# Kernel optimization log

Measured on AMD Instinct MI355X. Metric: run time of the kernel, lower is better.

## Reference

```python
import jax, jax.numpy as jnp
import numpy as np

N = 8192
F_IN, HID, LAT = 256, 128, 32


def setup_inputs() -> dict:
    key = jax.random.key(0)
    k1, k2, k3, k4 = jax.random.split(key, 4)
    X = jax.random.normal(k1, (N, F_IN), dtype=jnp.float32)
    # Dense normalized-adjacency stand-in (original converts dense A_tilde to COO each call)
    A_tilde = jax.random.uniform(k2, (N, N), dtype=jnp.float32) / N
    # Xavier-uniform init like torch's init.xavier_uniform_ on Linear weights
    lim1 = float(np.sqrt(6.0 / (F_IN + HID)))
    lim2 = float(np.sqrt(6.0 / (HID + LAT)))
    W1 = jax.random.uniform(k3, (F_IN, HID), dtype=jnp.float32, minval=-lim1, maxval=lim1)
    W2 = jax.random.uniform(k4, (HID, LAT), dtype=jnp.float32, minval=-lim2, maxval=lim2)
    return {"X": X, "A_tilde": A_tilde, "W1": W1, "W2": W2}


def reference(X, A_tilde, W1, W2):
    # GCN layer 1: A_tilde @ (X W1), then ReLU
    h = jax.nn.relu(A_tilde @ (X @ W1))          # [N, HID]
    # GCN layer 2 (no activation)
    Z = A_tilde @ (h @ W2)                        # [N, LAT]
    # Inner-product decoder
    A_hat = jax.nn.sigmoid(Z @ Z.T)               # [N, N]
    return A_hat
```

## Files before the change

kernel.cpp:

```cpp
#include <hip/hip_runtime.h>
#include <hip/hip_bf16.h>

#define N_ 8192
#define F_ 256
#define H_ 128
#define L_ 32

typedef __attribute__((ext_vector_type(8))) short bf16x8;
typedef __attribute__((ext_vector_type(4))) float f32x4;
typedef __attribute__((ext_vector_type(4))) short bf16x4;

__device__ __forceinline__ unsigned f2bf_u(float x) {
    unsigned u = __builtin_bit_cast(unsigned, x);
    return (u + 0x7fffu + ((u >> 16) & 1u)) >> 16;
}
__device__ __forceinline__ short f2bf(float x) { return (short)f2bf_u(x); }

__device__ __forceinline__ bf16x8 cvt8(float4 a, float4 b) {
    bf16x8 v;
    v[0] = f2bf(a.x); v[1] = f2bf(a.y); v[2] = f2bf(a.z); v[3] = f2bf(a.w);
    v[4] = f2bf(b.x); v[5] = f2bf(b.y); v[6] = f2bf(b.z); v[7] = f2bf(b.w);
    return v;
}

__global__ __launch_bounds__(256) void k0_cvt(const float* __restrict__ A,
                                              short* __restrict__ Ab) {
    size_t g = ((size_t)blockIdx.x * 256 + threadIdx.x) * 8;
    float4 a = *(const float4*)(A + g);
    float4 b = *(const float4*)(A + g + 4);
    *(bf16x8*)(Ab + g) = cvt8(a, b);
}

__global__ __launch_bounds__(256) void k1_xw1(const float* __restrict__ X,
                                              const float* __restrict__ W1,
                                              short* __restrict__ XW1T) {
    __shared__ short w1t[H_ * (F_ + 8)];
    const int tid = threadIdx.x;
    for (int idx = tid; idx < F_ * H_; idx += 256) {
        int k = idx >> 7, n = idx & 127;
        w1t[n * (F_ + 8) + k] = f2bf(W1[idx]);
    }
    __syncthreads();
    const int wv = tid >> 6, l = tid & 63;
    const int lm = l & 15, q = l >> 4;
    const int i0 = blockIdx.x * 64 + wv * 16;
    const float* xrow = X + (size_t)(i0 + lm) * F_;
    f32x4 acc[8];
#pragma unroll
    for (int j = 0; j < 8; ++j) acc[j] = (f32x4){0.f, 0.f, 0.f, 0.f};
#pragma unroll
    for (int k0 = 0; k0 < F_; k0 += 32) {
        float4 a0 = *(const float4*)(xrow + k0 + q * 8);
        float4 a1 = *(const float4*)(xrow + k0 + q * 8 + 4);
        bf16x8 af = cvt8(a0, a1);
#pragma unroll
        for (int j = 0; j < 8; ++j) {
            bf16x8 bf = *(const bf16x8*)&w1t[(j * 16 + lm) * (F_ + 8) + k0 + q * 8];
            acc[j] = __builtin_amdgcn_mfma_f32_16x16x32_bf16(af, bf, acc[j], 0, 0, 0);
        }
    }
#pragma unroll
    for (int j = 0; j < 8; ++j) {
        bf16x4 o;
        o[0] = f2bf(acc[j][0]); o[1] = f2bf(acc[j][1]);
        o[2] = f2bf(acc[j][2]); o[3] = f2bf(acc[j][3]);
        *(bf16x4*)(XW1T + (size_t)(j * 16 + lm) * N_ + i0 + q * 4) = o;
    }
}

__global__ __launch_bounds__(256) void k2_h_zp(const short* __restrict__ Ab,
                                               const short* __restrict__ XW1T,
                                               const float* __restrict__ W2,
                                               short* __restrict__ ZPT) {
    __shared__ float lacc[4][16][132];
    __shared__ short hl[16][136];
    __shared__ short w2t[32][136];
    const int tid = threadIdx.x;
    for (int idx = tid; idx < H_ * L_; idx += 256) {
        int k = idx >> 5, j = idx & 31;
        w2t[j][k] = f2bf(W2[idx]);
    }
    const int wv = tid >> 6, l = tid & 63, lm = l & 15, q = l >> 4;
    const int i0 = blockIdx.x * 16;
    const int kbeg = wv * (N_ / 4);
    const short* Arow = Ab + (size_t)(i0 + lm) * N_ + kbeg + q * 8;
    const short* Bp[8];
#pragma unroll
    for (int jt = 0; jt < 8; ++jt)
        Bp[jt] = XW1T + (size_t)(jt * 16 + lm) * N_ + kbeg + q * 8;

    bf16x8 pa[2], pb[2][8];
#pragma unroll
    for (int t = 0; t < 2; ++t) {
        pa[t] = *(const bf16x8*)(Arow + t * 32);
#pragma unroll
        for (int jt = 0; jt < 8; ++jt) pb[t][jt] = *(const bf16x8*)(Bp[jt] + t * 32);
    }
    f32x4 acc[8];
#pragma unroll
    for (int j = 0; j < 8; ++j) acc[j] = (f32x4){0.f, 0.f, 0.f, 0.f};

    const int NS = (N_ / 4) / 32;
#pragma unroll 2
    for (int s = 0; s < NS; ++s) {
        const int p = s & 1;
        bf16x8 af = pa[p];
#pragma unroll
        for (int jt = 0; jt < 8; ++jt)
            acc[jt] = __builtin_amdgcn_mfma_f32_16x16x32_bf16(af, pb[p][jt], acc[jt], 0, 0, 0);
        if (s + 2 < NS) {
            pa[p] = *(const bf16x8*)(Arow + (s + 2) * 32);
#pragma unroll
            for (int jt = 0; jt < 8; ++jt)
                pb[p][jt] = *(const bf16x8*)(Bp[jt] + (s + 2) * 32);
        }
    }
#pragma unroll
    for (int jt = 0; jt < 8; ++jt)
#pragma unroll
        for (int r = 0; r < 4; ++r)
            lacc[wv][q * 4 + r][jt * 16 + lm] = acc[jt][r];
    __syncthreads();
    for (int e = tid; e < 16 * H_; e += 256) {
        int rr = e >> 7, c = e & 127;
        float v = (lacc[0][rr][c] + lacc[1][rr][c]) + (lacc[2][rr][c] + lacc[3][rr][c]);
        hl[rr][c] = f2bf(v > 0.f ? v : 0.f);
    }
    __syncthreads();
    if (wv < 2) {
        f32x4 a2 = (f32x4){0.f, 0.f, 0.f, 0.f};
#pragma unroll
        for (int k0 = 0; k0 < H_; k0 += 32) {
            bf16x8 af2 = *(const bf16x8*)&hl[lm][k0 + q * 8];
            bf16x8 bf2 = *(const bf16x8*)&w2t[wv * 16 + lm][k0 + q * 8];
            a2 = __builtin_amdgcn_mfma_f32_16x16x32_bf16(af2, bf2, a2, 0, 0, 0);
        }
        bf16x4 o;
        o[0] = f2bf(a2[0]); o[1] = f2bf(a2[1]); o[2] = f2bf(a2[2]); o[3] = f2bf(a2[3]);
        *(bf16x4*)(ZPT + (size_t)(wv * 16 + lm) * N_ + i0 + q * 4) = o;
    }
}

__global__ __launch_bounds__(256) void k3_z(const short* __restrict__ Ab,
                                            const short* __restrict__ ZPT,
                                            short* __restrict__ Z) {
    __shared__ float lacc[4][16][36];
    const int tid = threadIdx.x;
    const int wv = tid >> 6, l = tid & 63, lm = l & 15, q = l >> 4;
    const int i0 = blockIdx.x * 16;
    const int kbeg = wv * (N_ / 4);
    const short* Arow = Ab + (size_t)(i0 + lm) * N_ + kbeg + q * 8;
    const short* Bp0 = ZPT + (size_t)lm * N_ + kbeg + q * 8;
    const short* Bp1 = Bp0 + (size_t)16 * N_;

    bf16x8 pa[2], pb0[2], pb1[2];
#pragma unroll
    for (int t = 0; t < 2; ++t) {
        pa[t]  = *(const bf16x8*)(Arow + t * 32);
        pb0[t] = *(const bf16x8*)(Bp0 + t * 32);
        pb1[t] = *(const bf16x8*)(Bp1 + t * 32);
    }
    f32x4 acc0 = (f32x4){0.f, 0.f, 0.f, 0.f};
    f32x4 acc1 = (f32x4){0.f, 0.f, 0.f, 0.f};
    const int NS = (N_ / 4) / 32;
#pragma unroll 2
    for (int s = 0; s < NS; ++s) {
        const int p = s & 1;
        acc0 = __builtin_amdgcn_mfma_f32_16x16x32_bf16(pa[p], pb0[p], acc0, 0, 0, 0);
        acc1 = __builtin_amdgcn_mfma_f32_16x16x32_bf16(pa[p], pb1[p], acc1, 0, 0, 0);
        if (s + 2 < NS) {
            pa[p]  = *(const bf16x8*)(Arow + (s + 2) * 32);
            pb0[p] = *(const bf16x8*)(Bp0 + (s + 2) * 32);
            pb1[p] = *(const bf16x8*)(Bp1 + (s + 2) * 32);
        }
    }
#pragma unroll
    for (int r = 0; r < 4; ++r) {
        lacc[wv][q * 4 + r][lm]      = acc0[r];
        lacc[wv][q * 4 + r][16 + lm] = acc1[r];
    }
    __syncthreads();
    {
        int e = tid * 2;
        int rr = e >> 5, c = e & 31;
        float v0 = (lacc[0][rr][c] + lacc[1][rr][c]) + (lacc[2][rr][c] + lacc[3][rr][c]);
        float v1 = (lacc[0][rr][c + 1] + lacc[1][rr][c + 1]) + (lacc[2][rr][c + 1] + lacc[3][rr][c + 1]);
        unsigned pk = f2bf_u(v0) | (f2bf_u(v1) << 16);
        *(unsigned*)(Z + (size_t)(i0 + rr) * L_ + c) = pk;
    }
}

__global__ __launch_bounds__(256) void k4_dec(const short* __restrict__ Z,
                                              float* __restrict__ out) {
    __shared__ float os[128][132];
    const int tid = threadIdx.x;
    const int wv = tid >> 6, l = tid & 63;
    const int lm = l & 15, q = l >> 4;
    const int bj = blockIdx.x & 63, bi = blockIdx.x >> 6;
    const int i0 = bi * 128, j0 = bj * 128;
    bf16x8 af[2];
#pragma unroll
    for (int t = 0; t < 2; ++t)
        af[t] = *(const bf16x8*)(Z + (size_t)(i0 + wv * 32 + t * 16 + lm) * L_ + q * 8);
#pragma unroll
    for (int tj = 0; tj < 8; ++tj) {
        bf16x8 bfv = *(const bf16x8*)(Z + (size_t)(j0 + tj * 16 + lm) * L_ + q * 8);
#pragma unroll
        for (int t = 0; t < 2; ++t) {
            f32x4 c = __builtin_amdgcn_mfma_f32_16x16x32_bf16(
                af[t], bfv, (f32x4){0.f, 0.f, 0.f, 0.f}, 0, 0, 0);
#pragma unroll
            for (int r = 0; r < 4; ++r) {
                float e = __expf(-c[r]);
                os[wv * 32 + t * 16 + q * 4 + r][tj * 16 + lm] = __fdividef(1.f, 1.f + e);
            }
        }
    }
    __syncthreads();
    for (int idx = tid; idx < 128 * 32; idx += 256) {
        int row = idx >> 5, c4 = idx & 31;
        *(float4*)(out + (size_t)(i0 + row) * N_ + j0 + c4 * 4) = *(const float4*)&os[row][c4 * 4];
    }
}

extern "C" void kernel_launch(void* const* d_in, const int* in_sizes, int n_in,
                              void* d_out, int out_size, void* d_ws, size_t ws_size,
                              hipStream_t stream) {
    const float* X  = (const float*)d_in[0];
    const float* A  = (const float*)d_in[1];
    const float* W1 = (const float*)d_in[2];
    const float* W2 = (const float*)d_in[3];
    float* out = (float*)d_out;

    short* XW1T = (short*)d_ws;
    short* ZPT  = XW1T + (size_t)H_ * N_;
    short* Z    = ZPT + (size_t)L_ * N_;
    short* Ab   = Z + (size_t)N_ * L_;

    k1_xw1<<<N_ / 64, 256, 0, stream>>>(X, W1, XW1T);
    k0_cvt<<<(N_ * N_) / (256 * 8), 256, 0, stream>>>(A, Ab);
    k2_h_zp<<<N_ / 16, 256, 0, stream>>>(Ab, XW1T, W2, ZPT);
    k3_z<<<N_ / 16, 256, 0, stream>>>(Ab, ZPT, Z);
    k4_dec<<<(N_ / 128) * (N_ / 128), 256, 0, stream>>>(Z, out);
}
```

Before: 672.9 us.

## Fuse fp32-to-bf16 adjacency conversion into GCN aggregation kernels with LDS staging

Removes the separate kernel that converted the dense adjacency to bf16. The two aggregation kernels now read fp32 A directly, convert it in registers and stage it through double-buffered, XOR-swizzled LDS. Work is split by output columns across waves instead of splitting K and reducing through LDS. The decoder is restructured so each block writes full 16-row strips in 512-column chunks with prefetched B fragments. This saves writing and rereading a bf16 copy of A, but A is now read in fp32 twice, once per aggregation layer.

```diff
diff --git a/kernel.cpp b/kernel.cpp
--- a/kernel.cpp
+++ b/kernel.cpp
@@ -23,14 +23,6 @@
     return v;
 }
 
-__global__ __launch_bounds__(256) void k0_cvt(const float* __restrict__ A,
-                                              short* __restrict__ Ab) {
-    size_t g = ((size_t)blockIdx.x * 256 + threadIdx.x) * 8;
-    float4 a = *(const float4*)(A + g);
-    float4 b = *(const float4*)(A + g + 4);
-    *(bf16x8*)(Ab + g) = cvt8(a, b);
-}
-
 __global__ __launch_bounds__(256) void k1_xw1(const float* __restrict__ X,
                                               const float* __restrict__ W1,
                                               short* __restrict__ XW1T) {
@@ -68,11 +60,11 @@
     }
 }
 
-__global__ __launch_bounds__(256) void k2_h_zp(const short* __restrict__ Ab,
+__global__ __launch_bounds__(256) void k2_h_zp(const float* __restrict__ A,
                                                const short* __restrict__ XW1T,
                                                const float* __restrict__ W2,
                                                short* __restrict__ ZPT) {
-    __shared__ float lacc[4][16][132];
+    __shared__ short As[2][16 * 512];
     __shared__ short hl[16][136];
     __shared__ short w2t[32][136];
     const int tid = threadIdx.x;
@@ -82,50 +74,77 @@
     }
     const int wv = tid >> 6, l = tid & 63, lm = l & 15, q = l >> 4;
     const int i0 = blockIdx.x * 16;
-    const int kbeg = wv * (N_ / 4);
-    const short* Arow = Ab + (size_t)(i0 + lm) * N_ + kbeg + q * 8;
-    const short* Bp[8];
-#pragma unroll
-    for (int jt = 0; jt < 8; ++jt)
-        Bp[jt] = XW1T + (size_t)(jt * 16 + lm) * N_ + kbeg + q * 8;
-
-    bf16x8 pa[2], pb[2][8];
-#pragma unroll
-    for (int t = 0; t < 2; ++t) {
-        pa[t] = *(const bf16x8*)(Arow + t * 32);
-#pragma unroll
-        for (int jt = 0; jt < 8; ++jt) pb[t][jt] = *(const bf16x8*)(Bp[jt] + t * 32);
-    }
-    f32x4 acc[8];
-#pragma unroll
-    for (int j = 0; j < 8; ++j) acc[j] = (f32x4){0.f, 0.f, 0.f, 0.f};
-
-    const int NS = (N_ / 4) / 32;
-#pragma unroll 2
-    for (int s = 0; s < NS; ++s) {
-        const int p = s & 1;
-        bf16x8 af = pa[p];
-#pragma unroll
-        for (int jt = 0; jt < 8; ++jt)
-            acc[jt] = __builtin_amdgcn_mfma_f32_16x16x32_bf16(af, pb[p][jt], acc[jt], 0, 0, 0);
-        if (s + 2 < NS) {
-            pa[p] = *(const bf16x8*)(Arow + (s + 2) * 32);
-#pragma unroll
-            for (int jt = 0; jt < 8; ++jt)
-                pb[p][jt] = *(const bf16x8*)(Bp[jt] + (s + 2) * 32);
-        }
-    }
-#pragma unroll
-    for (int jt = 0; jt < 8; ++jt)
-#pragma unroll
-        for (int r = 0; r < 4; ++r)
-            lacc[wv][q * 4 + r][jt * 16 + lm] = acc[jt][r];
-    __syncthreads();
-    for (int e = tid; e < 16 * H_; e += 256) {
-        int rr = e >> 7, c = e & 127;
-        float v = (lacc[0][rr][c] + lacc[1][rr][c]) + (lacc[2][rr][c] + lacc[3][rr][c]);
-        hl[rr][c] = f2bf(v > 0.f ? v : 0.f);
-    }
+    const int srow = tid >> 4, scol = (tid & 15) * 8;
+    const int sswz = (srow & 7) * 8;
+    const float* Ap = A + (size_t)(i0 + srow) * N_ + scol;
+    const short* Bp0 = XW1T + (size_t)(wv * 32 + lm) * N_ + q * 8;
+    const short* Bp1 = XW1T + (size_t)(wv * 32 + 16 + lm) * N_ + q * 8;
+
+    bf16x8 pb[2][2];
+    pb[0][0] = *(const bf16x8*)(Bp0);      pb[0][1] = *(const bf16x8*)(Bp1);
+    pb[1][0] = *(const bf16x8*)(Bp0 + 32); pb[1][1] = *(const bf16x8*)(Bp1 + 32);
+
+    float4 sa[8];
+#pragma unroll
+    for (int r = 0; r < 4; ++r) {
+        sa[2 * r]     = *(const float4*)(Ap + r * 128);
+        sa[2 * r + 1] = *(const float4*)(Ap + r * 128 + 4);
+    }
+#pragma unroll
+    for (int r = 0; r < 4; ++r) {
+        int col = scol + r * 128;
+        *(bf16x8*)&As[0][srow * 512 + (col ^ sswz)] = cvt8(sa[2 * r], sa[2 * r + 1]);
+    }
+#pragma unroll
+    for (int r = 0; r < 4; ++r) {
+        sa[2 * r]     = *(const float4*)(Ap + 512 + r * 128);
+        sa[2 * r + 1] = *(const float4*)(Ap + 512 + r * 128 + 4);
+    }
+    __syncthreads();
+
+    f32x4 acc[2];
+    acc[0] = (f32x4){0.f, 0.f, 0.f, 0.f};
+    acc[1] = (f32x4){0.f, 0.f, 0.f, 0.f};
+    const int fswz = (lm & 7) * 8;
+    const int NSTEP = N_ / 512;
+    for (int s = 0; s < NSTEP; ++s) {
+        const int b = s & 1;
+#pragma unroll
+        for (int m = 0; m < 16; ++m) {
+            const int gm = s * 16 + m;
+            const int col = m * 32 + q * 8;
+            bf16x8 af = *(const bf16x8*)&As[b][lm * 512 + (col ^ fswz)];
+            const int slot = gm & 1;
+            bf16x8 b0 = pb[slot][0], b1 = pb[slot][1];
+            pb[slot][0] = *(const bf16x8*)(Bp0 + (size_t)(gm + 2) * 32);
+            pb[slot][1] = *(const bf16x8*)(Bp1 + (size_t)(gm + 2) * 32);
+            acc[0] = __builtin_amdgcn_mfma_f32_16x16x32_bf16(af, b0, acc[0], 0, 0, 0);
+            acc[1] = __builtin_amdgcn_mfma_f32_16x16x32_bf16(af, b1, acc[1], 0, 0, 0);
+        }
+        if (s + 1 < NSTEP) {
+            const int nb = (s + 1) & 1;
+#pragma unroll
+            for (int r = 0; r < 4; ++r) {
+                int col = scol + r * 128;
+                *(bf16x8*)&As[nb][srow * 512 + (col ^ sswz)] = cvt8(sa[2 * r], sa[2 * r + 1]);
+            }
+            if (s + 2 < NSTEP) {
+#pragma unroll
+                for (int r = 0; r < 4; ++r) {
+                    sa[2 * r]     = *(const float4*)(Ap + (size_t)(s + 2) * 512 + r * 128);
+                    sa[2 * r + 1] = *(const float4*)(Ap + (size_t)(s + 2) * 512 + r * 128 + 4);
+                }
+            }
+        }
+        __syncthreads();
+    }
+#pragma unroll
+    for (int jt = 0; jt < 2; ++jt)
+#pragma unroll
+        for (int r = 0; r < 4; ++r) {
+            float v = acc[jt][r];
+            hl[q * 4 + r][wv * 32 + jt * 16 + lm] = f2bf(v > 0.f ? v : 0.f);
+        }
     __syncthreads();
     if (wv < 2) {
         f32x4 a2 = (f32x4){0.f, 0.f, 0.f, 0.f};
@@ -141,85 +160,121 @@
     }
 }
 
-__global__ __launch_bounds__(256) void k3_z(const short* __restrict__ Ab,
+__global__ __launch_bounds__(256) void k3_z(const float* __restrict__ A,
                                             const short* __restrict__ ZPT,
                                             short* __restrict__ Z) {
-    __shared__ float lacc[4][16][36];
+    __shared__ short As[2][32 * 256];
     const int tid = threadIdx.x;
     const int wv = tid >> 6, l = tid & 63, lm = l & 15, q = l >> 4;
-    const int i0 = blockIdx.x * 16;
-    const int kbeg = wv * (N_ / 4);
-    const short* Arow = Ab + (size_t)(i0 + lm) * N_ + kbeg + q * 8;
-    const short* Bp0 = ZPT + (size_t)lm * N_ + kbeg + q * 8;
-    const short* Bp1 = Bp0 + (size_t)16 * N_;
-
-    bf16x8 pa[2], pb0[2], pb1[2];
-#pragma unroll
-    for (int t = 0; t < 2; ++t) {
-        pa[t]  = *(const bf16x8*)(Arow + t * 32);
-        pb0[t] = *(const bf16x8*)(Bp0 + t * 32);
-        pb1[t] = *(const bf16x8*)(Bp1 + t * 32);
-    }
-    f32x4 acc0 = (f32x4){0.f, 0.f, 0.f, 0.f};
-    f32x4 acc1 = (f32x4){0.f, 0.f, 0.f, 0.f};
-    const int NS = (N_ / 4) / 32;
-#pragma unroll 2
-    for (int s = 0; s < NS; ++s) {
-        const int p = s & 1;
-        acc0 = __builtin_amdgcn_mfma_f32_16x16x32_bf16(pa[p], pb0[p], acc0, 0, 0, 0);
-        acc1 = __builtin_amdgcn_mfma_f32_16x16x32_bf16(pa[p], pb1[p], acc1, 0, 0, 0);
-        if (s + 2 < NS) {
-            pa[p]  = *(const bf16x8*)(Arow + (s + 2) * 32);
-            pb0[p] = *(const bf16x8*)(Bp0 + (s + 2) * 32);
-            pb1[p] = *(const bf16x8*)(Bp1 + (s + 2) * 32);
-        }
-    }
-#pragma unroll
-    for (int r = 0; r < 4; ++r) {
-        lacc[wv][q * 4 + r][lm]      = acc0[r];
-        lacc[wv][q * 4 + r][16 + lm] = acc1[r];
-    }
-    __syncthreads();
-    {
-        int e = tid * 2;
-        int rr = e >> 5, c = e & 31;
-        float v0 = (lacc[0][rr][c] + lacc[1][rr][c]) + (lacc[2][rr][c] + lacc[3][rr][c]);
-        float v1 = (lacc[0][rr][c + 1] + lacc[1][rr][c + 1]) + (lacc[2][rr][c + 1] + lacc[3][rr][c + 1]);
-        unsigned pk = f2bf_u(v0) | (f2bf_u(v1) << 16);
-        *(unsigned*)(Z + (size_t)(i0 + rr) * L_ + c) = pk;
-    }
+    const int rs = (wv >> 1) & 1, jt = wv & 1;
+    const int i0 = blockIdx.x * 32;
+    const int srow = tid >> 3, scol = (tid & 7) * 8;
+    const int sswz = (srow & 7) * 8;
+    const float* Ap = A + (size_t)(i0 + srow) * N_ + scol;
+    const short* Bp = ZPT + (size_t)(jt * 16 + lm) * N_ + q * 8;
+
+    bf16x8 pb[2];
+    pb[0] = *(const bf16x8*)(Bp);
+    pb[1] = *(const bf16x8*)(Bp + 32);
+
+    float4 sa[8];
+#pragma unroll
+    for (int r = 0; r < 4; ++r) {
+        sa[2 * r]     = *(const float4*)(Ap + r * 64);
+        sa[2 * r + 1] = *(const float4*)(Ap + r * 64 + 4);
+    }
+#pragma unroll
+    for (int r = 0; r < 4; ++r) {
+        int col = scol + r * 64;
+        *(bf16x8*)&As[0][srow * 256 + (col ^ sswz)] = cvt8(sa[2 * r], sa[2 * r + 1]);
+    }
+#pragma unroll
+    for (int r = 0; r < 4; ++r) {
+        sa[2 * r]     = *(const float4*)(Ap + 256 + r * 64);
+        sa[2 * r + 1] = *(const float4*)(Ap + 256 + r * 64 + 4);
+    }
+    __syncthreads();
+
+    f32x4 acc = (f32x4){0.f, 0.f, 0.f, 0.f};
+    const int frow = rs * 16 + lm;
+    const int fswz = (lm & 7) * 8;
+    const int NSTEP = N_ / 256;
+    for (int s = 0; s < NSTEP; ++s) {
+        const int b = s & 1;
+#pragma unroll
+        for (int m = 0; m < 8; ++m) {
+            const int gm = s * 8 + m;
+            const int col = m * 32 + q * 8;
+            bf16x8 af = *(const bf16x8*)&As[b][frow * 256 + (col ^ fswz)];
+            const int slot = gm & 1;
+            bf16x8 bb = pb[slot];
+            pb[slot] = *(const bf16x8*)(Bp + (size_t)(gm + 2) * 32);
+            acc = __builtin_amdgcn_mfma_f32_16x16x32_bf16(af, bb, acc, 0, 0, 0);
+        }
+        if (s + 1 < NSTEP) {
+            const int nb = (s + 1) & 1;
+#pragma unroll
+            for (int r = 0; r < 4; ++r) {
+                int col = scol + r * 64;
+                *(bf16x8*)&As[nb][srow * 256 + (col ^ sswz)] = cvt8(sa[2 * r], sa[2 * r + 1]);
+            }
+            if (s + 2 < NSTEP) {
+#pragma unroll
+                for (int r = 0; r < 4; ++r) {
+                    sa[2 * r]     = *(const float4*)(Ap + (size_t)(s + 2) * 256 + r * 64);
+                    sa[2 * r + 1] = *(const float4*)(Ap + (size_t)(s + 2) * 256 + r * 64 + 4);
+                }
+            }
+        }
+        __syncthreads();
+    }
+#pragma unroll
+    for (int r = 0; r < 4; ++r)
+        Z[(size_t)(i0 + rs * 16 + q * 4 + r) * L_ + jt * 16 + lm] = f2bf(acc[r]);
 }
 
 __global__ __launch_bounds__(256) void k4_dec(const short* __restrict__ Z,
                                               float* __restrict__ out) {
-    __shared__ float os[128][132];
+    __shared__ float os[16][524];
     const int tid = threadIdx.x;
     const int wv = tid >> 6, l = tid & 63;
     const int lm = l & 15, q = l >> 4;
-    const int bj = blockIdx.x & 63, bi = blockIdx.x >> 6;
-    const int i0 = bi * 128, j0 = bj * 128;
-    bf16x8 af[2];
-#pragma unroll
-    for (int t = 0; t < 2; ++t)
-        af[t] = *(const bf16x8*)(Z + (size_t)(i0 + wv * 32 + t * 16 + lm) * L_ + q * 8);
-#pragma unroll
-    for (int tj = 0; tj < 8; ++tj) {
-        bf16x8 bfv = *(const bf16x8*)(Z + (size_t)(j0 + tj * 16 + lm) * L_ + q * 8);
-#pragma unroll
-        for (int t = 0; t < 2; ++t) {
+    const int i0 = blockIdx.x * 16;
+    const bf16x8 af = *(const bf16x8*)(Z + (size_t)(i0 + lm) * L_ + q * 8);
+    const short* Bbase = Z + q * 8;
+
+    bf16x8 pb[2];
+    pb[0] = *(const bf16x8*)(Bbase + (size_t)(wv * 128 + lm) * L_);
+    pb[1] = *(const bf16x8*)(Bbase + (size_t)(wv * 128 + 16 + lm) * L_);
+
+    const int srow = tid >> 4, sc = (tid & 15) * 4;
+    for (int rd = 0; rd < 16; ++rd) {
+#pragma unroll
+        for (int t = 0; t < 8; ++t) {
+            const int gt = rd * 8 + t;
+            const int slot = gt & 1;
+            bf16x8 bb = pb[slot];
+            const int nt = gt + 2;
+            const int nrd = nt >> 3, ntt = nt & 7;
+            pb[slot] = *(const bf16x8*)(Bbase + (size_t)(nrd * 512 + wv * 128 + ntt * 16 + lm) * L_);
             f32x4 c = __builtin_amdgcn_mfma_f32_16x16x32_bf16(
-                af[t], bfv, (f32x4){0.f, 0.f, 0.f, 0.f}, 0, 0, 0);
+                af, bb, (f32x4){0.f, 0.f, 0.f, 0.f}, 0, 0, 0);
 #pragma unroll
             for (int r = 0; r < 4; ++r) {
                 float e = __expf(-c[r]);
-                os[wv * 32 + t * 16 + q * 4 + r][tj * 16 + lm] = __fdividef(1.f, 1.f + e);
-            }
-        }
-    }
-    __syncthreads();
-    for (int idx = tid; idx < 128 * 32; idx += 256) {
-        int row = idx >> 5, c4 = idx & 31;
-        *(float4*)(out + (size_t)(i0 + row) * N_ + j0 + c4 * 4) = *(const float4*)&os[row][c4 * 4];
+                os[q * 4 + r][wv * 128 + t * 16 + lm] = __fdividef(1.f, 1.f + e);
+            }
+        }
+        __syncthreads();
+        {
+            float* orow = out + (size_t)(i0 + srow) * N_ + rd * 512;
+#pragma unroll
+            for (int rr = 0; rr < 8; ++rr) {
+                int col = sc + rr * 64;
+                *(float4*)(orow + col) = *(const float4*)&os[srow][col];
+            }
+        }
+        __syncthreads();
     }
 }
 
@@ -235,11 +290,9 @@
     short* XW1T = (short*)d_ws;
     short* ZPT  = XW1T + (size_t)H_ * N_;
     short* Z    = ZPT + (size_t)L_ * N_;
-    short* Ab   = Z + (size_t)N_ * L_;
 
     k1_xw1<<<N_ / 64, 256, 0, stream>>>(X, W1, XW1T);
-    k0_cvt<<<(N_ * N_) / (256 * 8), 256, 0, stream>>>(A, Ab);
-    k2_h_zp<<<N_ / 16, 256, 0, stream>>>(Ab, XW1T, W2, ZPT);
-    k3_z<<<N_ / 16, 256, 0, stream>>>(Ab, ZPT, Z);
-    k4_dec<<<(N_ / 128) * (N_ / 128), 256, 0, stream>>>(Z, out);
-}
+    k2_h_zp<<<N_ / 16, 256, 0, stream>>>(A, XW1T, W2, ZPT);
+    k3_z<<<N_ / 32, 256, 0, stream>>>(A, ZPT, Z);
+    k4_dec<<<N_ / 16, 256, 0, stream>>>(Z, out);
+}
```

Result: faster. 603.2 us (-10.4%).
